# Optimization experiments

Hardware: AMD Instinct MI355X
Metric: run time of the kernel (lower is better)

## Reference

```python
import jax, jax.numpy as jnp
import numpy as np

B, S = 8, 2048
CHANNELS, DIM, HEADS = 256, 3, 6
TCH = CHANNELS * 2  # 512
EPS = 1e-5


def _linear_init(key, out_f, in_f):
    # torch nn.Linear default init: U(-1/sqrt(in_f), 1/sqrt(in_f)) for W and b
    k1, k2 = jax.random.split(key)
    bound = 1.0 / np.sqrt(in_f)
    w = jax.random.uniform(k1, (out_f, in_f), jnp.float32, -bound, bound)
    b = jax.random.uniform(k2, (out_f,), jnp.float32, -bound, bound)
    return w, b


def setup_inputs() -> dict:
    key = jax.random.key(0)
    ks = jax.random.split(key, 8)
    x = jax.random.normal(ks[0], (B, S, TCH), jnp.float32)
    wq, bq = _linear_init(ks[1], DIM, TCH)
    wk, bk = _linear_init(ks[2], DIM, TCH)
    wv, bv = _linear_init(ks[3], DIM, TCH)
    wo, bo = _linear_init(ks[4], TCH, HEADS * DIM)
    w1, b1 = _linear_init(ks[5], TCH, TCH)
    w2, b2 = _linear_init(ks[6], TCH, TCH)
    gamma = jnp.ones((TCH,), jnp.float32)
    beta = jnp.zeros((TCH,), jnp.float32)
    return {"x": x, "wq": wq, "bq": bq, "wk": wk, "bk": bk, "wv": wv, "bv": bv,
            "wo": wo, "bo": bo, "w1": w1, "b1": b1, "w2": w2, "b2": b2,
            "gamma": gamma, "beta": beta}


def _layernorm(x, gamma, beta):
    mu = jnp.mean(x, axis=-1, keepdims=True)
    var = jnp.mean(jnp.square(x - mu), axis=-1, keepdims=True)
    return (x - mu) * jax.lax.rsqrt(var + EPS) * gamma + beta


def reference(x, wq, bq, wk, bk, wv, bv, wo, bo, w1, b1, w2, b2, gamma, beta):
    # All heads share the same w_q/w_k/w_v, so one attention pass suffices;
    # concatenating HEADS copies reproduces the original math exactly.
    q = x @ wq.T + bq                      # [B,S,DIM]
    k = x @ wk.T + bk                      # [B,S,DIM]
    v = x @ wv.T + bv                      # [B,S,DIM]
    scores = jnp.einsum('bqd,bkd->bqk', q, k) / np.sqrt(DIM)  # [B,S,S]
    soft = jax.nn.softmax(scores, axis=-1)
    z = jnp.einsum('bqk,bkd->bqd', soft, v)  # [B,S,DIM]
    z = jnp.concatenate([z] * HEADS, axis=-1)  # [B,S,HEADS*DIM]
    z = z @ wo.T + bo                       # [B,S,TCH]
    r0 = x + (z @ w1.T + b1)
    r1 = _layernorm(r0, gamma, beta)
    r1 = r1 @ w2.T + b2
    r = r0 + r1
    return _layernorm(r, gamma, beta)
```

## Files before the change

### kernel.cpp

```cpp
#include <hip/hip_runtime.h>
#include <hip/hip_bf16.h>

#define TCH 512
#define MTOT 16384
#define SEQ 2048
#define LN_EPS 1e-5f

typedef __attribute__((ext_vector_type(8))) __bf16 bf16x8;
typedef __attribute__((ext_vector_type(4))) float f32x4;

__device__ __forceinline__ unsigned pkbf(float a, float b) {
  union { __hip_bfloat16 h; unsigned short u; } ca, cb;
  ca.h = __float2bfloat16(a); cb.h = __float2bfloat16(b);
  return (unsigned)ca.u | ((unsigned)cb.u << 16);
}
__device__ __forceinline__ float bf_lo(unsigned u) { return __uint_as_float(u << 16); }
__device__ __forceinline__ float bf_hi(unsigned u) { return __uint_as_float(u & 0xffff0000u); }

__device__ __forceinline__ bf16x8 cvt8(float4 a, float4 b) {
  union { __hip_bfloat16 h; __bf16 v; } u;
  bf16x8 r;
  u.h = __float2bfloat16(a.x); r[0] = u.v;
  u.h = __float2bfloat16(a.y); r[1] = u.v;
  u.h = __float2bfloat16(a.z); r[2] = u.v;
  u.h = __float2bfloat16(a.w); r[3] = u.v;
  u.h = __float2bfloat16(b.x); r[4] = u.v;
  u.h = __float2bfloat16(b.y); r[5] = u.v;
  u.h = __float2bfloat16(b.z); r[6] = u.v;
  u.h = __float2bfloat16(b.w); r[7] = u.v;
  return r;
}

#define QSCALE 0.8329517853860118f

__global__ __launch_bounds__(256) void prep_kernel(
    const float* __restrict__ w2,
    const float* __restrict__ wo, const float* __restrict__ bo,
    const float* __restrict__ wq, const float* __restrict__ bq,
    const float* __restrict__ wk, const float* __restrict__ bk,
    const float* __restrict__ wv, const float* __restrict__ bv,
    const float* __restrict__ w1, const float* __restrict__ b1,
    __hip_bfloat16* __restrict__ w2b,
    __hip_bfloat16* __restrict__ wqkvb, float* __restrict__ qkvbias,
    float4* __restrict__ weff4)
{
  int i = blockIdx.x * 256 + threadIdx.x;
  w2b[i] = __float2bfloat16(w2[i]);
  if (i < 16 * TCH) {
    int row = i >> 9, k = i & 511;
    float v;
    if      (row < 3) v = wq[row * TCH + k] * QSCALE;
    else if (row < 6) v = wk[(row - 3) * TCH + k];
    else if (row < 9) v = wv[(row - 6) * TCH + k];
    else              v = 0.f;
    wqkvb[i] = __float2bfloat16(v);
  }
  if (i < 16) {
    float v;
    if      (i < 3) v = bq[i] * QSCALE;
    else if (i < 6) v = bk[i - 3];
    else if (i < 9) v = bv[i - 6];
    else            v = 0.f;
    qkvbias[i] = v;
  }
  if (blockIdx.x < 128) {
    const int t = threadIdx.x, w = t >> 6, l = t & 63;
    const int row = blockIdx.x * 4 + w;
    float sx = 0.f, sy = 0.f, sz = 0.f, sw = 0.f;
    #pragma unroll
    for (int j = 0; j < 8; ++j) {
      const int k = j * 64 + l;
      float e0 = 0.f, e1 = 0.f, e2 = 0.f;
      #pragma unroll
      for (int h = 0; h < 6; ++h) {
        e0 += wo[k*18 + h*3 + 0];
        e1 += wo[k*18 + h*3 + 1];
        e2 += wo[k*18 + h*3 + 2];
      }
      const float a = w1[(size_t)row * TCH + k];
      sx += a * e0; sy += a * e1; sz += a * e2; sw += a * bo[k];
    }
    #pragma unroll
    for (int off = 1; off < 64; off <<= 1) {
      sx += __shfl_xor(sx, off, 64);
      sy += __shfl_xor(sy, off, 64);
      sz += __shfl_xor(sz, off, 64);
      sw += __shfl_xor(sw, off, 64);
    }
    if (l == 0) weff4[row] = make_float4(sx, sy, sz, sw + b1[row]);
  }
}

__global__ __launch_bounds__(256) void qkv_kernel(
    const float* __restrict__ x,
    const __hip_bfloat16* __restrict__ wqkvb, const float* __restrict__ qkvbias,
    float4* __restrict__ q4, uint4* __restrict__ kvp)
{
  const int t = threadIdx.x, wv = t >> 6, ln = t & 63;
  const int l16 = ln & 15, quad = ln >> 4;
  const int row0 = blockIdx.x * 16;
  const int k0 = wv * 128;

  bf16x8 bfr[4];
  #pragma unroll
  for (int ks = 0; ks < 4; ++ks)
    bfr[ks] = *reinterpret_cast<const bf16x8*>(wqkvb + l16 * TCH + k0 + ks * 32 + quad * 8);

  const float* xp = x + (size_t)(row0 + l16) * TCH + k0 + quad * 8;

  f32x4 acc = {};
  #pragma unroll
  for (int ks = 0; ks < 4; ++ks) {
    float4 a = *(const float4*)(xp + ks * 32);
    float4 b = *(const float4*)(xp + ks * 32 + 4);
    acc = __builtin_amdgcn_mfma_f32_16x16x32_bf16(cvt8(a, b), bfr[ks], acc, 0, 0, 0);
  }

  __shared__ float tr[4][16][17];
  __shared__ float fin[16][17];
  #pragma unroll
  for (int r = 0; r < 4; ++r) tr[wv][quad * 4 + r][l16] = acc[r];
  __syncthreads();

  {
    const int r = t >> 4, c = t & 15;
    fin[r][c] = tr[0][r][c] + tr[1][r][c] + tr[2][r][c] + tr[3][r][c] + qkvbias[c];
  }
  __syncthreads();

  if (t < 16) {
    q4[row0 + t] = make_float4(fin[t][0], fin[t][1], fin[t][2], 0.f);
  } else if (t < 32) {
    const int r = t - 16;
    kvp[row0 + r] = make_uint4(pkbf(fin[r][3], fin[r][4]),
                               pkbf(fin[r][5], fin[r][6]),
                               pkbf(fin[r][7], fin[r][8]), 0u);
  }
}

__global__ __launch_bounds__(512) void attn_kernel(
    const float4* __restrict__ q4, const uint4* __restrict__ kvp,
    const float* __restrict__ x, const float4* __restrict__ weff4,
    const float* __restrict__ gamma, const float* __restrict__ beta,
    __hip_bfloat16* __restrict__ r0b, __hip_bfloat16* __restrict__ r1b)
{
  __shared__ float4 part[8 * 64];
  __shared__ float4 zbuf[64];

  const int b    = blockIdx.x >> 5;
  const int qc   = blockIdx.x & 31;
  const int base = b * SEQ;
  const int tid  = threadIdx.x;
  const int wave = tid >> 6;
  const int lane = tid & 63;
  const float4 q = q4[base + qc * 64 + lane];

  const int wu = __builtin_amdgcn_readfirstlane(wave);
  const uint4* kvw = kvp + base + wu * 256;

  float l[4] = {}, a0[4] = {}, a1[4] = {}, a2[4] = {};
  #pragma unroll 2
  for (int i = 0; i < 64; ++i) {
    #pragma unroll
    for (int s = 0; s < 4; ++s) {
      uint4 rec = kvw[s * 64 + i];
      float sc = bf_lo(rec.x) * q.x + bf_hi(rec.x) * q.y + bf_lo(rec.y) * q.z;
      float p = __builtin_amdgcn_exp2f(sc);
      l[s]  += p;
      a0[s] += p * bf_hi(rec.y);
      a1[s] += p * bf_lo(rec.z);
      a2[s] += p * bf_hi(rec.z);
    }
  }
  part[wave * 64 + lane] = make_float4(l[0]+l[1]+l[2]+l[3],
                                       a0[0]+a0[1]+a0[2]+a0[3],
                                       a1[0]+a1[1]+a1[2]+a1[3],
                                       a2[0]+a2[1]+a2[2]+a2[3]);
  __syncthreads();

  if (tid < 64) {
    float L = 0.f, A0 = 0.f, A1 = 0.f, A2 = 0.f;
    #pragma unroll
    for (int w = 0; w < 8; ++w) {
      float4 p = part[w * 64 + tid];
      L += p.x; A0 += p.y; A1 += p.z; A2 += p.w;
    }
    const float inv = 1.f / L;
    zbuf[tid] = make_float4(A0 * inv, A1 * inv, A2 * inv, 0.f);
  }
  __syncthreads();

  const int c0 = lane * 8;
  float4 wvv[8];
  #pragma unroll
  for (int j = 0; j < 8; ++j) wvv[j] = weff4[c0 + j];
  const float4 g0  = *(const float4*)(gamma + c0);
  const float4 g1  = *(const float4*)(gamma + c0 + 4);
  const float4 be0 = *(const float4*)(beta  + c0);
  const float4 be1 = *(const float4*)(beta  + c0 + 4);
  const float gg[8] = {g0.x,g0.y,g0.z,g0.w,g1.x,g1.y,g1.z,g1.w};
  const float bb[8] = {be0.x,be0.y,be0.z,be0.w,be1.x,be1.y,be1.z,be1.w};

  #pragma unroll
  for (int qi = 0; qi < 8; ++qi) {
    const int qloc = wave * 8 + qi;
    const int grow = base + qc * 64 + qloc;
    const float4 z = zbuf[qloc];
    const float* xr = x + (size_t)grow * TCH + c0;
    const float4 x0 = *(const float4*)xr;
    const float4 x1 = *(const float4*)(xr + 4);
    const float xv[8] = {x0.x,x0.y,x0.z,x0.w,x1.x,x1.y,x1.z,x1.w};
    float r0v[8], s = 0.f, sq = 0.f;
    #pragma unroll
    for (int j = 0; j < 8; ++j) {
      float v = xv[j] + z.x * wvv[j].x + z.y * wvv[j].y + z.z * wvv[j].z + wvv[j].w;
      r0v[j] = v; s += v; sq += v * v;
    }
    #pragma unroll
    for (int off = 1; off < 64; off <<= 1) {
      s  += __shfl_xor(s,  off, 64);
      sq += __shfl_xor(sq, off, 64);
    }
    const float mu = s * (1.f / TCH);
    const float rs = rsqrtf(sq * (1.f / TCH) - mu * mu + LN_EPS);
    *(bf16x8*)(r0b + (size_t)grow * TCH + c0) =
        cvt8(make_float4(r0v[0], r0v[1], r0v[2], r0v[3]),
             make_float4(r0v[4], r0v[5], r0v[6], r0v[7]));
    float r1v[8];
    #pragma unroll
    for (int j = 0; j < 8; ++j) r1v[j] = (r0v[j] - mu) * rs * gg[j] + bb[j];
    *(bf16x8*)(r1b + (size_t)grow * TCH + c0) =
        cvt8(make_float4(r1v[0], r1v[1], r1v[2], r1v[3]),
             make_float4(r1v[4], r1v[5], r1v[6], r1v[7]));
  }
}

__global__ __launch_bounds__(256) void gemm_kernel(
    const __hip_bfloat16* __restrict__ A,
    const __hip_bfloat16* __restrict__ W,
    const float* __restrict__ bias,
    const __hip_bfloat16* __restrict__ res,
    __hip_bfloat16* __restrict__ Cout,
    float2* __restrict__ partial)
{
  __shared__ __align__(16) __hip_bfloat16 At[2][4][128][8];
  __shared__ __align__(16) __hip_bfloat16 Wt[2][4][128][8];
  __shared__ float redS[128][2];
  __shared__ float redQ[128][2];

  const int bx   = blockIdx.x;
  const int rb   = bx & 127, cb = bx >> 7;
  const int row0 = rb * 128, col0 = cb * 128;
  const int t    = threadIdx.x;
  const int w    = t >> 6, l = t & 63;
  const int l16  = l & 15, quad = l >> 4;
  const int wr   = w >> 1, wc = w & 1;
  const int srow = t & 127;
  const int sq0  = (t >> 7) << 1;

  auto stage = [&](int ks, int b) {
    #pragma unroll
    for (int j = 0; j < 2; ++j) {
      const int q = sq0 | j;
      __builtin_amdgcn_global_load_lds(
          (const __attribute__((address_space(1))) void*)(A + (size_t)(row0 + srow) * TCH + ks * 32 + q * 8),
          (__attribute__((address_space(3))) void*)&At[b][q][srow][0], 16, 0, 0);
      __builtin_amdgcn_global_load_lds(
          (const __attribute__((address_space(1))) void*)(W + (size_t)(col0 + srow) * TCH + ks * 32 + q * 8),
          (__attribute__((address_space(3))) void*)&Wt[b][q][srow][0], 16, 0, 0);
    }
  };

  f32x4 acc[4][4] = {};
  stage(0, 0);
  for (int ks = 0; ks < 16; ++ks) {
    const int cur = ks & 1;
    __syncthreads();
    if (ks < 15) stage(ks + 1, cur ^ 1);
    bf16x8 af[4], bf[4];
    #pragma unroll
    for (int mt = 0; mt < 4; ++mt)
      af[mt] = *reinterpret_cast<const bf16x8*>(&At[cur][quad][wr * 64 + mt * 16 + l16][0]);
    #pragma unroll
    for (int nt = 0; nt < 4; ++nt)
      bf[nt] = *reinterpret_cast<const bf16x8*>(&Wt[cur][quad][wc * 64 + nt * 16 + l16][0]);
    #pragma unroll
    for (int mt = 0; mt < 4; ++mt)
      #pragma unroll
      for (int nt = 0; nt < 4; ++nt)
        acc[mt][nt] = __builtin_amdgcn_mfma_f32_16x16x32_bf16(af[mt], bf[nt], acc[mt][nt], 0, 0, 0);
  }

  #pragma unroll
  for (int mt = 0; mt < 4; ++mt) {
    #pragma unroll
    for (int r = 0; r < 4; ++r) {
      const int lrow = wr * 64 + mt * 16 + quad * 4 + r;
      const int grow = row0 + lrow;
      float s = 0.f, sq = 0.f;
      #pragma unroll
      for (int nt = 0; nt < 4; ++nt) {
        const int col = col0 + wc * 64 + nt * 16 + l16;
        float v = acc[mt][nt][r] + bias[col] + __bfloat162float(res[(size_t)grow * TCH + col]);
        Cout[(size_t)grow * TCH + col] = __float2bfloat16(v);
        s += v; sq += v * v;
      }
      #pragma unroll
      for (int off = 1; off < 16; off <<= 1) {
        s  += __shfl_xor(s,  off, 64);
        sq += __shfl_xor(sq, off, 64);
      }
      if (l16 == 0) { redS[lrow][wc] = s; redQ[lrow][wc] = sq; }
    }
  }
  __syncthreads();

  if (t < 128) {
    partial[(size_t)cb * MTOT + row0 + t] =
        make_float2(redS[t][0] + redS[t][1], redQ[t][0] + redQ[t][1]);
  }
}

template<typename OUT_T>
__global__ __launch_bounds__(256) void ln_kernel(
    const __hip_bfloat16* __restrict__ Cin, const float2* __restrict__ partial,
    const float* __restrict__ gamma, const float* __restrict__ beta,
    OUT_T* __restrict__ out)
{
  const int t = threadIdx.x, wv = t >> 6, ln = t & 63;
  const int row = blockIdx.x * 4 + wv;

  float2 p0 = partial[row];
  float2 p1 = partial[MTOT + row];
  float2 p2 = partial[2 * MTOT + row];
  float2 p3 = partial[3 * MTOT + row];
  const float S = p0.x + p1.x + p2.x + p3.x;
  const float Q = p0.y + p1.y + p2.y + p3.y;
  const float mu  = S * (1.f / TCH);
  const float var = Q * (1.f / TCH) - mu * mu;
  const float rs  = rsqrtf(var + LN_EPS);

  const int c0 = ln * 8;
  bf16x8 vr = *reinterpret_cast<const bf16x8*>(Cin + (size_t)row * TCH + c0);
  float4 g0 = *(const float4*)(gamma + c0), g1 = *(const float4*)(gamma + c0 + 4);
  float4 b0 = *(const float4*)(beta  + c0), b1 = *(const float4*)(beta  + c0 + 4);

  float o[8];
  const float gg[8] = {g0.x,g0.y,g0.z,g0.w,g1.x,g1.y,g1.z,g1.w};
  const float bb[8] = {b0.x,b0.y,b0.z,b0.w,b1.x,b1.y,b1.z,b1.w};
  #pragma unroll
  for (int j = 0; j < 8; ++j) {
    union { __bf16 v; __hip_bfloat16 h; } u; u.v = vr[j];
    o[j] = (__bfloat162float(u.h) - mu) * rs * gg[j] + bb[j];
  }

  if constexpr (sizeof(OUT_T) == 2) {
    unsigned ov[4];
    #pragma unroll
    for (int j = 0; j < 4; ++j) ov[j] = pkbf(o[2*j], o[2*j+1]);
    *(uint4*)((__hip_bfloat16*)out + (size_t)row * TCH + c0) =
        make_uint4(ov[0], ov[1], ov[2], ov[3]);
  } else {
    float* op = (float*)out + (size_t)row * TCH + c0;
    *(float4*)op       = make_float4(o[0], o[1], o[2], o[3]);
    *(float4*)(op + 4) = make_float4(o[4], o[5], o[6], o[7]);
  }
}

extern "C" void kernel_launch(void* const* d_in, const int* in_sizes, int n_in,
                              void* d_out, int out_size, void* d_ws, size_t ws_size,
                              hipStream_t stream) {
  (void)in_sizes; (void)n_in; (void)out_size; (void)ws_size;
  const float* x     = (const float*)d_in[0];
  const float* wq    = (const float*)d_in[1];
  const float* bq    = (const float*)d_in[2];
  const float* wk    = (const float*)d_in[3];
  const float* bk    = (const float*)d_in[4];
  const float* wv    = (const float*)d_in[5];
  const float* bv    = (const float*)d_in[6];
  const float* wo    = (const float*)d_in[7];
  const float* bo    = (const float*)d_in[8];
  const float* w1    = (const float*)d_in[9];
  const float* b1    = (const float*)d_in[10];
  const float* w2    = (const float*)d_in[11];
  const float* b2    = (const float*)d_in[12];
  const float* gamma = (const float*)d_in[13];
  const float* beta  = (const float*)d_in[14];
  float* out = (float*)d_out;

  char* ws = (char*)d_ws;
  size_t off = 0;
  float4* q4      = (float4*)(ws + off); off += (size_t)MTOT * 16;
  uint4*  kvp     = (uint4*)(ws + off);  off += (size_t)MTOT * 16;
  float4* weff4   = (float4*)(ws + off); off += (size_t)TCH * 16;
  __hip_bfloat16* w2b   = (__hip_bfloat16*)(ws + off); off += (size_t)TCH * TCH * 2;
  __hip_bfloat16* wqkvb = (__hip_bfloat16*)(ws + off); off += (size_t)16 * TCH * 2;
  float*          qkvbias = (float*)(ws + off);        off += 64;
  __hip_bfloat16* r0b = (__hip_bfloat16*)(ws + off); off += (size_t)MTOT * TCH * 2;
  __hip_bfloat16* r1b = (__hip_bfloat16*)(ws + off); off += (size_t)MTOT * TCH * 2;
  __hip_bfloat16* rrb = (__hip_bfloat16*)(ws + off); off += (size_t)MTOT * TCH * 2;
  float2* part2 = (float2*)(ws + off); off += (size_t)4 * MTOT * 8;

  prep_kernel<<<(TCH*TCH)/256, 256, 0, stream>>>(
      w2, wo, bo, wq, bq, wk, bk, wv, bv, w1, b1, w2b, wqkvb, qkvbias, weff4);
  qkv_kernel<<<MTOT/16, 256, 0, stream>>>(x, wqkvb, qkvbias, q4, kvp);
  attn_kernel<<<MTOT/64, 512, 0, stream>>>(q4, kvp, x, weff4, gamma, beta, r0b, r1b);
  gemm_kernel<<<512, 256, 0, stream>>>(r1b, w2b, b2, r0b, rrb, part2);
  ln_kernel<float><<<MTOT/4, 256, 0, stream>>>(rrb, part2, gamma, beta, out);
}
```

Measured before the change: 180.9 us.

## Fuse final LayerNorm into GEMM via last-block counter and double K-step

Removes the separate ln_kernel launch. Each GEMM block atomically bumps a per-row-block counter, and the last of the four column blocks to finish applies the final LayerNorm to its 128 rows, reading the partial sums and bf16 results written by its peers. The GEMM K-tile is also widened from 32 to 64 per stage, which halves the barrier and stage count. The cost is a serialized LN tail run by one block per row group, plus more LDS per block, which may lower occupancy.

```diff
diff --git a/kernel.cpp b/kernel.cpp
--- a/kernel.cpp
+++ b/kernel.cpp
@@ -42,10 +42,11 @@
     const float* __restrict__ w1, const float* __restrict__ b1,
     __hip_bfloat16* __restrict__ w2b,
     __hip_bfloat16* __restrict__ wqkvb, float* __restrict__ qkvbias,
-    float4* __restrict__ weff4)
+    float4* __restrict__ weff4, int* __restrict__ cnt)
 {
   int i = blockIdx.x * 256 + threadIdx.x;
   w2b[i] = __float2bfloat16(w2[i]);
+  if (blockIdx.x == 1023 && threadIdx.x < 128) cnt[threadIdx.x] = 0;
   if (i < 16 * TCH) {
     int row = i >> 9, k = i & 511;
     float v;
@@ -241,12 +242,16 @@
     const float* __restrict__ bias,
     const __hip_bfloat16* __restrict__ res,
     __hip_bfloat16* __restrict__ Cout,
-    float2* __restrict__ partial)
+    float2* __restrict__ partial,
+    int* __restrict__ cnt,
+    const float* __restrict__ gamma, const float* __restrict__ beta,
+    float* __restrict__ out)
 {
-  __shared__ __align__(16) __hip_bfloat16 At[2][4][128][8];
-  __shared__ __align__(16) __hip_bfloat16 Wt[2][4][128][8];
+  __shared__ __align__(16) __hip_bfloat16 At[2][8][128][8];
+  __shared__ __align__(16) __hip_bfloat16 Wt[2][8][128][8];
   __shared__ float redS[128][2];
   __shared__ float redQ[128][2];
+  __shared__ int lastS;
 
   const int bx   = blockIdx.x;
   const int rb   = bx & 127, cb = bx >> 7;
@@ -256,39 +261,43 @@
   const int l16  = l & 15, quad = l >> 4;
   const int wr   = w >> 1, wc = w & 1;
   const int srow = t & 127;
-  const int sq0  = (t >> 7) << 1;
-
-  auto stage = [&](int ks, int b) {
-    #pragma unroll
-    for (int j = 0; j < 2; ++j) {
-      const int q = sq0 | j;
+  const int qb   = (t >> 7) * 4;
+
+  auto stage = [&](int kb, int b) {
+    #pragma unroll
+    for (int j = 0; j < 4; ++j) {
+      const int q = qb + j;
       __builtin_amdgcn_global_load_lds(
-          (const __attribute__((address_space(1))) void*)(A + (size_t)(row0 + srow) * TCH + ks * 32 + q * 8),
+          (const __attribute__((address_space(1))) void*)(A + (size_t)(row0 + srow) * TCH + kb * 64 + q * 8),
           (__attribute__((address_space(3))) void*)&At[b][q][srow][0], 16, 0, 0);
       __builtin_amdgcn_global_load_lds(
-          (const __attribute__((address_space(1))) void*)(W + (size_t)(col0 + srow) * TCH + ks * 32 + q * 8),
+          (const __attribute__((address_space(1))) void*)(W + (size_t)(col0 + srow) * TCH + kb * 64 + q * 8),
           (__attribute__((address_space(3))) void*)&Wt[b][q][srow][0], 16, 0, 0);
     }
   };
 
   f32x4 acc[4][4] = {};
   stage(0, 0);
-  for (int ks = 0; ks < 16; ++ks) {
-    const int cur = ks & 1;
+  for (int kb = 0; kb < 8; ++kb) {
+    const int cur = kb & 1;
     __syncthreads();
-    if (ks < 15) stage(ks + 1, cur ^ 1);
-    bf16x8 af[4], bf[4];
-    #pragma unroll
-    for (int mt = 0; mt < 4; ++mt)
-      af[mt] = *reinterpret_cast<const bf16x8*>(&At[cur][quad][wr * 64 + mt * 16 + l16][0]);
-    #pragma unroll
-    for (int nt = 0; nt < 4; ++nt)
-      bf[nt] = *reinterpret_cast<const bf16x8*>(&Wt[cur][quad][wc * 64 + nt * 16 + l16][0]);
-    #pragma unroll
-    for (int mt = 0; mt < 4; ++mt)
+    if (kb < 7) stage(kb + 1, cur ^ 1);
+    #pragma unroll
+    for (int s = 0; s < 2; ++s) {
+      const int kq = s * 4 + quad;
+      bf16x8 af[4], bf[4];
+      #pragma unroll
+      for (int mt = 0; mt < 4; ++mt)
+        af[mt] = *reinterpret_cast<const bf16x8*>(&At[cur][kq][wr * 64 + mt * 16 + l16][0]);
       #pragma unroll
       for (int nt = 0; nt < 4; ++nt)
-        acc[mt][nt] = __builtin_amdgcn_mfma_f32_16x16x32_bf16(af[mt], bf[nt], acc[mt][nt], 0, 0, 0);
+        bf[nt] = *reinterpret_cast<const bf16x8*>(&Wt[cur][kq][wc * 64 + nt * 16 + l16][0]);
+      #pragma unroll
+      for (int mt = 0; mt < 4; ++mt)
+        #pragma unroll
+        for (int nt = 0; nt < 4; ++nt)
+          acc[mt][nt] = __builtin_amdgcn_mfma_f32_16x16x32_bf16(af[mt], bf[nt], acc[mt][nt], 0, 0, 0);
+    }
   }
 
   #pragma unroll
@@ -319,51 +328,42 @@
     partial[(size_t)cb * MTOT + row0 + t] =
         make_float2(redS[t][0] + redS[t][1], redQ[t][0] + redQ[t][1]);
   }
-}
-
-template<typename OUT_T>
-__global__ __launch_bounds__(256) void ln_kernel(
-    const __hip_bfloat16* __restrict__ Cin, const float2* __restrict__ partial,
-    const float* __restrict__ gamma, const float* __restrict__ beta,
-    OUT_T* __restrict__ out)
-{
-  const int t = threadIdx.x, wv = t >> 6, ln = t & 63;
-  const int row = blockIdx.x * 4 + wv;
-
-  float2 p0 = partial[row];
-  float2 p1 = partial[MTOT + row];
-  float2 p2 = partial[2 * MTOT + row];
-  float2 p3 = partial[3 * MTOT + row];
-  const float S = p0.x + p1.x + p2.x + p3.x;
-  const float Q = p0.y + p1.y + p2.y + p3.y;
-  const float mu  = S * (1.f / TCH);
-  const float var = Q * (1.f / TCH) - mu * mu;
-  const float rs  = rsqrtf(var + LN_EPS);
-
-  const int c0 = ln * 8;
-  bf16x8 vr = *reinterpret_cast<const bf16x8*>(Cin + (size_t)row * TCH + c0);
-  float4 g0 = *(const float4*)(gamma + c0), g1 = *(const float4*)(gamma + c0 + 4);
-  float4 b0 = *(const float4*)(beta  + c0), b1 = *(const float4*)(beta  + c0 + 4);
-
-  float o[8];
-  const float gg[8] = {g0.x,g0.y,g0.z,g0.w,g1.x,g1.y,g1.z,g1.w};
-  const float bb[8] = {b0.x,b0.y,b0.z,b0.w,b1.x,b1.y,b1.z,b1.w};
-  #pragma unroll
-  for (int j = 0; j < 8; ++j) {
-    union { __bf16 v; __hip_bfloat16 h; } u; u.v = vr[j];
-    o[j] = (__bfloat162float(u.h) - mu) * rs * gg[j] + bb[j];
-  }
-
-  if constexpr (sizeof(OUT_T) == 2) {
-    unsigned ov[4];
-    #pragma unroll
-    for (int j = 0; j < 4; ++j) ov[j] = pkbf(o[2*j], o[2*j+1]);
-    *(uint4*)((__hip_bfloat16*)out + (size_t)row * TCH + c0) =
-        make_uint4(ov[0], ov[1], ov[2], ov[3]);
-  } else {
-    float* op = (float*)out + (size_t)row * TCH + c0;
-    *(float4*)op       = make_float4(o[0], o[1], o[2], o[3]);
-    *(float4*)(op + 4) = make_float4(o[4], o[5], o[6], o[7]);
+  __syncthreads();
+
+  if (t == 0) {
+    __threadfence();
+    lastS = (atomicAdd(&cnt[rb], 1) == 3) ? 1 : 0;
+  }
+  __syncthreads();
+
+  if (lastS) {
+    __threadfence();
+    const int c0 = l * 8;
+    const float4 g0 = *(const float4*)(gamma + c0), g1 = *(const float4*)(gamma + c0 + 4);
+    const float4 b0 = *(const float4*)(beta  + c0), b1 = *(const float4*)(beta  + c0 + 4);
+    const float gg[8] = {g0.x,g0.y,g0.z,g0.w,g1.x,g1.y,g1.z,g1.w};
+    const float bbv[8] = {b0.x,b0.y,b0.z,b0.w,b1.x,b1.y,b1.z,b1.w};
+    for (int rr = 0; rr < 32; ++rr) {
+      const int row = row0 + w * 32 + rr;
+      const float2 p0 = partial[row];
+      const float2 p1 = partial[MTOT + row];
+      const float2 p2 = partial[2 * MTOT + row];
+      const float2 p3 = partial[3 * MTOT + row];
+      const float S = p0.x + p1.x + p2.x + p3.x;
+      const float Q = p0.y + p1.y + p2.y + p3.y;
+      const float mu = S * (1.f / TCH);
+      const float rs = rsqrtf(Q * (1.f / TCH) - mu * mu + LN_EPS);
+      bf16x8 vr = *reinterpret_cast<const bf16x8*>(Cout + (size_t)row * TCH + c0);
+      float o[8];
+      #pragma unroll
+      for (int j = 0; j < 8; ++j) {
+        union { __bf16 v; __hip_bfloat16 h; } u; u.v = vr[j];
+        o[j] = (__bfloat162float(u.h) - mu) * rs * gg[j] + bbv[j];
+      }
+      float* op = out + (size_t)row * TCH + c0;
+      *(float4*)op       = make_float4(o[0], o[1], o[2], o[3]);
+      *(float4*)(op + 4) = make_float4(o[4], o[5], o[6], o[7]);
+    }
   }
 }
 
@@ -396,15 +396,15 @@
   __hip_bfloat16* w2b   = (__hip_bfloat16*)(ws + off); off += (size_t)TCH * TCH * 2;
   __hip_bfloat16* wqkvb = (__hip_bfloat16*)(ws + off); off += (size_t)16 * TCH * 2;
   float*          qkvbias = (float*)(ws + off);        off += 64;
+  int*            cnt     = (int*)(ws + off);          off += 512;
   __hip_bfloat16* r0b = (__hip_bfloat16*)(ws + off); off += (size_t)MTOT * TCH * 2;
   __hip_bfloat16* r1b = (__hip_bfloat16*)(ws + off); off += (size_t)MTOT * TCH * 2;
   __hip_bfloat16* rrb = (__hip_bfloat16*)(ws + off); off += (size_t)MTOT * TCH * 2;
   float2* part2 = (float2*)(ws + off); off += (size_t)4 * MTOT * 8;
 
   prep_kernel<<<(TCH*TCH)/256, 256, 0, stream>>>(
-      w2, wo, bo, wq, bq, wk, bk, wv, bv, w1, b1, w2b, wqkvb, qkvbias, weff4);
+      w2, wo, bo, wq, bq, wk, bk, wv, bv, w1, b1, w2b, wqkvb, qkvbias, weff4, cnt);
   qkv_kernel<<<MTOT/16, 256, 0, stream>>>(x, wqkvb, qkvbias, q4, kvp);
   attn_kernel<<<MTOT/64, 512, 0, stream>>>(q4, kvp, x, weff4, gamma, beta, r0b, r1b);
-  gemm_kernel<<<512, 256, 0, stream>>>(r1b, w2b, b2, r0b, rrb, part2);
-  ln_kernel<float><<<MTOT/4, 256, 0, stream>>>(rrb, part2, gamma, beta, out);
-}
+  gemm_kernel<<<512, 256, 0, stream>>>(r1b, w2b, b2, r0b, rrb, part2, cnt, gamma, beta, out);
+}
```

After: 210.1 us. 16.2% more time.
